# Kernel tuning notes

Hardware: AMD Instinct MI355X
Metric: run time of the kernel (lower is better)

## Reference

```python
import jax, jax.numpy as jnp
import numpy as np

N = 100000   # nodes
E = 300000   # directed edges
IN_DIM = 10
HID = 384
OUT_DIM = 3
T = 5
BN_EPS = 1e-5


def setup_inputs() -> dict:
    key = jax.random.key(0)
    ks = jax.random.split(key, 32)
    i = iter(range(32))
    nxt = lambda: ks[next(i)]
    d = {}
    d["x"] = jax.random.normal(nxt(), (N, IN_DIM), dtype=jnp.float32)
    d["edge_index"] = jax.random.randint(nxt(), (2, E), 0, N, dtype=jnp.int32)
    s = 0.05
    # SAGEConv layer 0 (in_dim -> hid); lin_l has bias, lin_r has no bias (PyG defaults)
    d["W_l0"] = jax.random.normal(nxt(), (HID, IN_DIM), dtype=jnp.float32) * s
    d["b_l0"] = jnp.zeros((HID,), dtype=jnp.float32)
    d["W_r0"] = jax.random.normal(nxt(), (HID, IN_DIM), dtype=jnp.float32) * s
    # SAGEConv layers 1..T-1 (hid -> hid), stacked
    d["W_l"] = jax.random.normal(nxt(), (T - 1, HID, HID), dtype=jnp.float32) * s
    d["b_l"] = jnp.zeros((T - 1, HID), dtype=jnp.float32)
    d["W_r"] = jax.random.normal(nxt(), (T - 1, HID, HID), dtype=jnp.float32) * s
    # per-layer BatchNorm (eval mode: running stats)
    d["bn_g"] = jnp.ones((T, HID), dtype=jnp.float32)
    d["bn_b"] = jnp.zeros((T, HID), dtype=jnp.float32)
    d["bn_m"] = jax.random.normal(nxt(), (T, HID), dtype=jnp.float32) * 0.1
    d["bn_v"] = jax.random.uniform(nxt(), (T, HID), dtype=jnp.float32, minval=0.5, maxval=1.5)
    # projection MLP: Linear->BN->ReLU->Linear->BN->ReLU->Linear
    d["Wp0"] = jax.random.normal(nxt(), (HID, HID), dtype=jnp.float32) * s
    d["bp0"] = jnp.zeros((HID,), dtype=jnp.float32)
    d["Wp1"] = jax.random.normal(nxt(), (HID, HID), dtype=jnp.float32) * s
    d["bp1"] = jnp.zeros((HID,), dtype=jnp.float32)
    d["Wp2"] = jax.random.normal(nxt(), (OUT_DIM, HID), dtype=jnp.float32) * s
    d["bp2"] = jnp.zeros((OUT_DIM,), dtype=jnp.float32)
    d["pbn_g"] = jnp.ones((2, HID), dtype=jnp.float32)
    d["pbn_b"] = jnp.zeros((2, HID), dtype=jnp.float32)
    d["pbn_m"] = jax.random.normal(nxt(), (2, HID), dtype=jnp.float32) * 0.1
    d["pbn_v"] = jax.random.uniform(nxt(), (2, HID), dtype=jnp.float32, minval=0.5, maxval=1.5)
    return d


def _bn(x, g, b, m, v):
    return (x - m) * jax.lax.rsqrt(v + BN_EPS) * g + b


def _sage(x, src, dst, Wl, bl, Wr):
    # mean aggregation of neighbor features, then lin_l(agg) + lin_r(x), L2-normalized
    msg = jax.ops.segment_sum(x[src], dst, num_segments=N)            # [N, F]
    cnt = jax.ops.segment_sum(jnp.ones_like(dst, dtype=x.dtype), dst, num_segments=N)
    agg = msg / jnp.maximum(cnt, 1.0)[:, None]
    out = agg @ Wl.T + bl + x @ Wr.T
    nrm = jnp.linalg.norm(out, axis=-1, keepdims=True)
    return out / jnp.maximum(nrm, 1e-12)


def reference(x, edge_index, W_l0, b_l0, W_r0, W_l, b_l, W_r,
              bn_g, bn_b, bn_m, bn_v,
              Wp0, bp0, Wp1, bp1, Wp2, bp2,
              pbn_g, pbn_b, pbn_m, pbn_v):
    src, dst = edge_index[0], edge_index[1]
    h = x
    for t in range(T):  # T=5, fixed small loop over structurally distinct layers
        if t == 0:
            h = _sage(h, src, dst, W_l0, b_l0, W_r0)
        else:
            h = _sage(h, src, dst, W_l[t - 1], b_l[t - 1], W_r[t - 1])
        h = jax.nn.elu(_bn(h, bn_g[t], bn_b[t], bn_m[t], bn_v[t]))
        # dropout is identity in eval mode
    # projection MLP
    h = jax.nn.relu(_bn(h @ Wp0.T + bp0, pbn_g[0], pbn_b[0], pbn_m[0], pbn_v[0]))
    h = jax.nn.relu(_bn(h @ Wp1.T + bp1, pbn_g[1], pbn_b[1], pbn_m[1], pbn_v[1]))
    return h @ Wp2.T + bp2  # [N, 3]
```

## Files before the change

### kernel.cpp

```cpp
#include <hip/hip_runtime.h>
#include <hip/hip_bf16.h>

#define N_NODES 100000
#define N_EDGES 300000
#define IN_DIM 10
#define HID 384
#define OUT_DIM 3
#define T_LAYERS 5
#define BN_EPS 1e-5f

typedef __attribute__((ext_vector_type(8))) short short8;
typedef __attribute__((ext_vector_type(4))) float floatx4;

__device__ __forceinline__ float bf16f(short v) {
  return __uint_as_float(((unsigned)(unsigned short)v) << 16);
}

__device__ __forceinline__ void gld_lds16(const void* g, void* l) {
  __builtin_amdgcn_global_load_lds(
      (const __attribute__((address_space(1))) void*)g,
      (__attribute__((address_space(3))) void*)l, 16, 0, 0);
}


__global__ void count_k(const int* __restrict__ dst, int* __restrict__ cnt, int E) {
  int e = blockIdx.x * blockDim.x + threadIdx.x;
  if (e < E) atomicAdd(&cnt[dst[e]], 1);
}

__global__ void scan_partial_k(const int* __restrict__ cnt, int* __restrict__ bsum, int n) {
  int t = threadIdx.x;
  int i = blockIdx.x * 1024 + t;
  int v = (i < n) ? cnt[i] : 0;
  #pragma unroll
  for (int off = 1; off < 64; off <<= 1) v += __shfl_xor(v, off);
  __shared__ int ws[16];
  if ((t & 63) == 0) ws[t >> 6] = v;
  __syncthreads();
  if (t == 0) {
    int s = 0;
    #pragma unroll
    for (int w = 0; w < 16; ++w) s += ws[w];
    bsum[blockIdx.x] = s;
  }
}

__global__ void scan_small_k(int* __restrict__ bsum, int P) {
  __shared__ int s[1024];
  int t = threadIdx.x;
  int v = (t < P) ? bsum[t] : 0;
  s[t] = v;
  __syncthreads();
  for (int off = 1; off < 1024; off <<= 1) {
    int add = (t >= off) ? s[t - off] : 0;
    __syncthreads();
    s[t] += add;
    __syncthreads();
  }
  if (t < P) bsum[t] = s[t] - v;
}

__global__ void scan_final_k(const int* __restrict__ cnt, const int* __restrict__ bsum,
                             int* __restrict__ row_off, int n) {
  int t = threadIdx.x, lane = t & 63, wv = t >> 6;
  int i = blockIdx.x * 1024 + t;
  int v = (i < n) ? cnt[i] : 0;
  int x = v;
  #pragma unroll
  for (int off = 1; off < 64; off <<= 1) {
    int y = __shfl_up(x, off);
    if (lane >= off) x += y;
  }
  __shared__ int ws[16];
  if (lane == 63) ws[wv] = x;
  __syncthreads();
  if (t == 0) {
    int a = 0;
    #pragma unroll
    for (int w = 0; w < 16; ++w) { int tmp = ws[w]; ws[w] = a; a += tmp; }
  }
  __syncthreads();
  int excl = (x - v) + ws[wv] + bsum[blockIdx.x];
  if (i <= n) row_off[i] = excl;
}

__global__ void fill_k(const int* __restrict__ src, const int* __restrict__ dst,
                       const int* __restrict__ row_off, int* __restrict__ cursor,
                       int* __restrict__ csr, int E) {
  int e = blockIdx.x * blockDim.x + threadIdx.x;
  if (e < E) {
    int d = dst[e];
    int pos = atomicAdd(&cursor[d], 1);
    csr[row_off[d] + pos] = src[e];
  }
}


__global__ void conv_k(const float* __restrict__ src, __hip_bfloat16* __restrict__ dst, int n) {
  int i = blockIdx.x * blockDim.x + threadIdx.x;
  if (i < n) dst[i] = __float2bfloat16(src[i]);
}

__global__ void pack0_k(const float* __restrict__ x, const float* __restrict__ agg10,
                        __hip_bfloat16* __restrict__ X2, int n) {
  int i = blockIdx.x * blockDim.x + threadIdx.x;
  if (i < n * 64) {
    int node = i >> 6, k = i & 63;
    float v = (k < IN_DIM) ? x[node * IN_DIM + k]
              : (k < 2 * IN_DIM) ? agg10[node * IN_DIM + (k - IN_DIM)] : 0.f;
    X2[i] = __float2bfloat16(v);
  }
}

__global__ void packw0_k(const float* __restrict__ Wl, const float* __restrict__ Wr,
                         __hip_bfloat16* __restrict__ W2) {
  int i = blockIdx.x * blockDim.x + threadIdx.x;
  if (i < HID * 64) {
    int o = i >> 6, k = i & 63;
    float v = (k < IN_DIM) ? Wr[o * IN_DIM + k]
              : (k < 2 * IN_DIM) ? Wl[o * IN_DIM + (k - IN_DIM)]
              : 0.f;
    W2[i] = __float2bfloat16(v);
  }
}


__global__ void agg10_k(const float* __restrict__ x, const int* __restrict__ row_off,
                        const int* __restrict__ csr, float* __restrict__ agg10, int n) {
  int sub = threadIdx.x >> 5;
  int lane = threadIdx.x & 31;
  int node = blockIdx.x * 8 + sub;
  if (node >= n) return;
  int s = row_off[node], e = row_off[node + 1];
  if (lane < IN_DIM) {
    float acc = 0.f;
    for (int j = s; j < e; ++j) acc += x[csr[j] * IN_DIM + lane];
    float c = (float)max(e - s, 1);
    agg10[node * IN_DIM + lane] = acc / c;
  }
}

__global__ __launch_bounds__(256) void aggv_k(const __hip_bfloat16* __restrict__ h,
                                              const int* __restrict__ row_off,
                                              const int* __restrict__ csr,
                                              __hip_bfloat16* __restrict__ agg, int n) {
  int node = blockIdx.x * 4 + (threadIdx.x >> 6);
  if (node >= n) return;
  int lane = threadIdx.x & 63;
  int s = row_off[node], e = row_off[node + 1];
  float a0 = 0.f, a1 = 0.f, a2 = 0.f, a3 = 0.f, a4 = 0.f, a5 = 0.f;
  const int doff = lane * 3;
  for (int j = s; j < e; ++j) {
    const uint* rp = (const uint*)(h + (size_t)csr[j] * HID) + doff;
    uint3 v = *(const uint3*)rp;
    a0 += __uint_as_float(v.x << 16);
    a1 += __uint_as_float(v.x & 0xffff0000u);
    a2 += __uint_as_float(v.y << 16);
    a3 += __uint_as_float(v.y & 0xffff0000u);
    a4 += __uint_as_float(v.z << 16);
    a5 += __uint_as_float(v.z & 0xffff0000u);
  }
  float invc = 1.f / (float)max(e - s, 1);
  __hip_bfloat16 b0 = __float2bfloat16(a0 * invc), b1 = __float2bfloat16(a1 * invc);
  __hip_bfloat16 b2 = __float2bfloat16(a2 * invc), b3 = __float2bfloat16(a3 * invc);
  __hip_bfloat16 b4 = __float2bfloat16(a4 * invc), b5 = __float2bfloat16(a5 * invc);
  uint o0 = (uint)(*(unsigned short*)&b0) | ((uint)(*(unsigned short*)&b1) << 16);
  uint o1 = (uint)(*(unsigned short*)&b2) | ((uint)(*(unsigned short*)&b3) << 16);
  uint o2 = (uint)(*(unsigned short*)&b4) | ((uint)(*(unsigned short*)&b5) << 16);
  *(uint3*)((uint*)(agg + (size_t)node * HID) + doff) = make_uint3(o0, o1, o2);
}

template <int KTOT, bool DUAL, int EPI, bool FINAL>
__global__ __launch_bounds__(512, 4) void mfma_gemm_k(
    const __hip_bfloat16* __restrict__ A1, const __hip_bfloat16* __restrict__ B1,
    const __hip_bfloat16* __restrict__ A2, const __hip_bfloat16* __restrict__ B2,
    const float* __restrict__ bias,
    const float* __restrict__ bng, const float* __restrict__ bnb,
    const float* __restrict__ bnm, const float* __restrict__ bnv,
    __hip_bfloat16* __restrict__ out,
    const float* __restrict__ W3, const float* __restrict__ b3,
    float* __restrict__ out3) {
  __shared__ alignas(16) short smem[32768];
  short* sB = smem + 8192;

  const int t = threadIdx.x;
  const int lane = t & 63;
  const int wv = t >> 6;
  const int n16 = lane & 15;
  const int quad = lane >> 4;
  const int row0 = blockIdx.x * 64;

  const int aRow = t >> 3;
  const int aG = (t & 7) ^ (aRow & 7);
  const int aOff = min(row0 + aRow, N_NODES - 1) * KTOT + aG * 8;
  const int bCol0 = wv * 48 + (lane >> 3);
  const int bG = (lane & 7) ^ ((lane >> 3) & 7);
  const int bOff0 = bCol0 * KTOT + bG * 8;

  floatx4 acc[4][3];
  #pragma unroll
  for (int rt = 0; rt < 4; ++rt)
    #pragma unroll
    for (int ct = 0; ct < 3; ++ct) acc[rt][ct] = (floatx4)0.f;

  constexpr int KCH = KTOT / 64;
  constexpr int NCH = DUAL ? 2 * KCH : KCH;

  gld_lds16(A1 + aOff, smem + wv * 512);

  for (int c = 0; c < NCH; ++c) {
    const __hip_bfloat16* Bp;
    int kc;
    if (!DUAL || c < KCH) { Bp = B1; kc = c * 64; }
    else                  { Bp = B2; kc = (c - KCH) * 64; }

    #pragma unroll
    for (int it = 0; it < 6; ++it)
      gld_lds16(Bp + bOff0 + (it * 8 * KTOT + kc), sB + (wv * 6 + it) * 512);

    if (c + 1 < NCH) {
      const __hip_bfloat16* Ap;
      int kn;
      int cn = c + 1;
      if (!DUAL || cn < KCH) { Ap = A1; kn = cn * 64; }
      else                   { Ap = A2; kn = (cn - KCH) * 64; }
      gld_lds16(Ap + aOff + kn, smem + (cn & 1) * 4096 + wv * 512);
      asm volatile("s_waitcnt vmcnt(1)" ::: "memory");
    } else {
      asm volatile("s_waitcnt vmcnt(0)" ::: "memory");
    }
    __builtin_amdgcn_sched_barrier(0);
    __builtin_amdgcn_s_barrier();

    const short* sAc = smem + (c & 1) * 4096;
    #pragma unroll
    for (int kh = 0; kh < 2; ++kh) {
      short8 af[4];
      int g = kh * 4 + quad;
      #pragma unroll
      for (int rt = 0; rt < 4; ++rt) {
        int r = rt * 16 + n16;
        af[rt] = *(const short8*)&sAc[r * 64 + ((g ^ (r & 7)) * 8)];
      }
      #pragma unroll
      for (int ct = 0; ct < 3; ++ct) {
        int cl = wv * 48 + ct * 16 + n16;
        short8 bf = *(const short8*)&sB[cl * 64 + ((g ^ (cl & 7)) * 8)];
        #pragma unroll
        for (int rt = 0; rt < 4; ++rt)
          acc[rt][ct] = __builtin_amdgcn_mfma_f32_16x16x32_bf16(af[rt], bf, acc[rt][ct], 0, 0, 0);
      }
    }
    __builtin_amdgcn_s_barrier();
    asm volatile("" ::: "memory");
  }

  const int gcBase = wv * 48 + n16;
  #pragma unroll
  for (int ct = 0; ct < 3; ++ct) {
    float bs = bias[gcBase + ct * 16];
    #pragma unroll
    for (int rt = 0; rt < 4; ++rt)
      #pragma unroll
      for (int rg = 0; rg < 4; ++rg) acc[rt][ct][rg] += bs;
  }

  if constexpr (EPI == 0) {
    float* red = (float*)smem;
    #pragma unroll
    for (int rt = 0; rt < 4; ++rt)
      #pragma unroll
      for (int rg = 0; rg < 4; ++rg) {
        float s = 0.f;
        #pragma unroll
        for (int ct = 0; ct < 3; ++ct) s += acc[rt][ct][rg] * acc[rt][ct][rg];
        #pragma unroll
        for (int off = 1; off < 16; off <<= 1) s += __shfl_xor(s, off);
        if (n16 == 0) red[wv * 64 + rt * 16 + quad * 4 + rg] = s;
      }
    __syncthreads();
    #pragma unroll
    for (int rt = 0; rt < 4; ++rt) {
      float inv[4];
      #pragma unroll
      for (int rg = 0; rg < 4; ++rg) {
        int rl = rt * 16 + quad * 4 + rg;
        float ss = 0.f;
        #pragma unroll
        for (int w = 0; w < 8; ++w) ss += red[w * 64 + rl];
        inv[rg] = rsqrtf(fmaxf(ss, 1e-24f));
      }
      #pragma unroll
      for (int ct = 0; ct < 3; ++ct)
        #pragma unroll
        for (int rg = 0; rg < 4; ++rg) acc[rt][ct][rg] *= inv[rg];
    }
    __syncthreads();
  }

  constexpr int OS = 392;
  short* sO = smem;
  #pragma unroll
  for (int ct = 0; ct < 3; ++ct) {
    int col = gcBase + ct * 16;
    float sc = bng[col] * rsqrtf(bnv[col] + BN_EPS);
    float sh = bnb[col] - bnm[col] * sc;
    #pragma unroll
    for (int rt = 0; rt < 4; ++rt)
      #pragma unroll
      for (int rg = 0; rg < 4; ++rg) {
        float xv = acc[rt][ct][rg] * sc + sh;
        if constexpr (EPI == 0)
          xv = xv > 0.f ? xv : (__expf(xv) - 1.0f);
        else
          xv = fmaxf(xv, 0.f);
        __hip_bfloat16 bv = __float2bfloat16(xv);
        sO[(rt * 16 + quad * 4 + rg) * OS + col] = *(short*)&bv;
      }
  }
  __syncthreads();

  if constexpr (FINAL) {
    if (t < 192) {
      int row = t & 63, o = t >> 6;
      int grow = row0 + row;
      if (grow < N_NODES) {
        float s = 0.f;
        #pragma unroll
        for (int kb = 0; kb < 48; ++kb) {
          short8 hv = *(const short8*)&sO[row * OS + kb * 8];
          #pragma unroll
          for (int j = 0; j < 8; ++j) s += bf16f(hv[j]) * W3[o * HID + kb * 8 + j];
        }
        out3[grow * OUT_DIM + o] = s + b3[o];
      }
    }
  } else {
    #pragma unroll
    for (int it = 0; it < 6; ++it) {
      int e = t + it * 512;
      int row = e / 48, cs = e % 48;
      int grow = row0 + row;
      if (grow < N_NODES) {
        uint4 v = *(const uint4*)&sO[row * OS + cs * 8];
        *(uint4*)(out + (size_t)grow * HID + cs * 8) = v;
      }
    }
  }
}


extern "C" void kernel_launch(void* const* d_in, const int* in_sizes, int n_in,
                              void* d_out, int out_size, void* d_ws, size_t ws_size,
                              hipStream_t stream) {
  const float* x = (const float*)d_in[0];
  const int* ei = (const int*)d_in[1];
  const int* src = ei;
  const int* dst = ei + N_EDGES;
  const float* W_l0 = (const float*)d_in[2];
  const float* b_l0 = (const float*)d_in[3];
  const float* W_r0 = (const float*)d_in[4];
  const float* W_l = (const float*)d_in[5];
  const float* b_l = (const float*)d_in[6];
  const float* W_r = (const float*)d_in[7];
  const float* bn_g = (const float*)d_in[8];
  const float* bn_b = (const float*)d_in[9];
  const float* bn_m = (const float*)d_in[10];
  const float* bn_v = (const float*)d_in[11];
  const float* Wp0 = (const float*)d_in[12];
  const float* bp0 = (const float*)d_in[13];
  const float* Wp1 = (const float*)d_in[14];
  const float* bp1 = (const float*)d_in[15];
  const float* Wp2 = (const float*)d_in[16];
  const float* bp2 = (const float*)d_in[17];
  const float* pbn_g = (const float*)d_in[18];
  const float* pbn_b = (const float*)d_in[19];
  const float* pbn_m = (const float*)d_in[20];
  const float* pbn_v = (const float*)d_in[21];

  char* ws = (char*)d_ws;
  size_t off = 0;
  auto walloc = [&](size_t bytes) -> void* {
    void* p = ws + off;
    off = (off + bytes + 255) & ~(size_t)255;
    return p;
  };
  __hip_bfloat16* h   = (__hip_bfloat16*)walloc((size_t)N_NODES * HID * 2);
  __hip_bfloat16* agg = (__hip_bfloat16*)walloc((size_t)N_NODES * HID * 2);
  float* agg10 = (float*)agg;
  __hip_bfloat16* X2  = (__hip_bfloat16*)walloc((size_t)N_NODES * 64 * 2);
  __hip_bfloat16* W2  = (__hip_bfloat16*)walloc((size_t)HID * 64 * 2);
  __hip_bfloat16* WlB  = (__hip_bfloat16*)walloc((size_t)(T_LAYERS - 1) * HID * HID * 2);
  __hip_bfloat16* WrB  = (__hip_bfloat16*)walloc((size_t)(T_LAYERS - 1) * HID * HID * 2);
  __hip_bfloat16* Wp0B = (__hip_bfloat16*)walloc((size_t)HID * HID * 2);
  __hip_bfloat16* Wp1B = (__hip_bfloat16*)walloc((size_t)HID * HID * 2);
  int* cnt     = (int*)walloc((size_t)N_NODES * 4);
  int* row_off = (int*)walloc((size_t)(N_NODES + 1) * 4);
  int* cursor  = (int*)walloc((size_t)N_NODES * 4);
  int* csr     = (int*)walloc((size_t)N_EDGES * 4);
  int* bsum    = (int*)walloc(4096);

  hipMemsetAsync(cnt, 0, (size_t)N_NODES * 4, stream);
  hipMemsetAsync(cursor, 0, (size_t)N_NODES * 4, stream);

  const int NW = (T_LAYERS - 1) * HID * HID;
  conv_k<<<(NW + 255) / 256, 256, 0, stream>>>(W_l, WlB, NW);
  conv_k<<<(NW + 255) / 256, 256, 0, stream>>>(W_r, WrB, NW);
  conv_k<<<(HID * HID + 255) / 256, 256, 0, stream>>>(Wp0, Wp0B, HID * HID);
  conv_k<<<(HID * HID + 255) / 256, 256, 0, stream>>>(Wp1, Wp1B, HID * HID);
  packw0_k<<<(HID * 64 + 255) / 256, 256, 0, stream>>>(W_l0, W_r0, W2);

  count_k<<<(N_EDGES + 255) / 256, 256, 0, stream>>>(dst, cnt, N_EDGES);
  int P = (N_NODES + 1 + 1023) / 1024;
  scan_partial_k<<<P, 1024, 0, stream>>>(cnt, bsum, N_NODES);
  scan_small_k<<<1, 1024, 0, stream>>>(bsum, P);
  scan_final_k<<<P, 1024, 0, stream>>>(cnt, bsum, row_off, N_NODES);
  fill_k<<<(N_EDGES + 255) / 256, 256, 0, stream>>>(src, dst, row_off, cursor, csr, N_EDGES);

  const int GB = (N_NODES + 63) / 64;

  agg10_k<<<(N_NODES + 7) / 8, 256, 0, stream>>>(x, row_off, csr, agg10, N_NODES);
  pack0_k<<<(N_NODES * 64 + 255) / 256, 256, 0, stream>>>(x, agg10, X2, N_NODES);
  mfma_gemm_k<64, false, 0, false><<<GB, 512, 0, stream>>>(
      X2, W2, nullptr, nullptr, b_l0, bn_g, bn_b, bn_m, bn_v, h,
      nullptr, nullptr, nullptr);

  for (int t = 1; t < T_LAYERS; ++t) {
    aggv_k<<<(N_NODES + 3) / 4, 256, 0, stream>>>(h, row_off, csr, agg, N_NODES);
    mfma_gemm_k<HID, true, 0, false><<<GB, 512, 0, stream>>>(
        agg, WlB + (size_t)(t - 1) * HID * HID,
        h,   WrB + (size_t)(t - 1) * HID * HID,
        b_l + (size_t)(t - 1) * HID,
        bn_g + (size_t)t * HID, bn_b + (size_t)t * HID,
        bn_m + (size_t)t * HID, bn_v + (size_t)t * HID,
        h, nullptr, nullptr, nullptr);
  }

  mfma_gemm_k<HID, false, 1, false><<<GB, 512, 0, stream>>>(
      h, Wp0B, nullptr, nullptr, bp0, pbn_g, pbn_b, pbn_m, pbn_v, h,
      nullptr, nullptr, nullptr);
  mfma_gemm_k<HID, false, 1, true><<<GB, 512, 0, stream>>>(
      h, Wp1B, nullptr, nullptr, bp1, pbn_g + HID, pbn_b + HID, pbn_m + HID, pbn_v + HID, h,
      Wp2, bp2, (float*)d_out);
}
```

Baseline: 910.2 us.

## Fuse projection MLP's two GEMMs and output layer into one kernel

Replaces the two separate projection GEMM launches with a single kernel that processes 128-row tiles with 1024 threads. The intermediate hidden activation stays in shared memory between the first GEMM, the second GEMM and the final 3-wide output. This removes a global write and re-read of the [N,384] bf16 intermediate and one launch. In exchange the kernel uses about 144 KB of LDS per block, which limits occupancy, and the second GEMM's B loads are not double-buffered.

```diff
diff --git a/kernel.cpp b/kernel.cpp
--- a/kernel.cpp
+++ b/kernel.cpp
@@ -345,6 +345,173 @@
         uint4 v = *(const uint4*)&sO[row * OS + cs * 8];
         *(uint4*)(out + (size_t)grow * HID + cs * 8) = v;
       }
+    }
+  }
+}
+
+__global__ __launch_bounds__(1024, 4) void proj_fused_k(
+    const __hip_bfloat16* __restrict__ h,
+    const __hip_bfloat16* __restrict__ B0, const __hip_bfloat16* __restrict__ B1,
+    const float* __restrict__ bias0, const float* __restrict__ bias1,
+    const float* __restrict__ pbn_g, const float* __restrict__ pbn_b,
+    const float* __restrict__ pbn_m, const float* __restrict__ pbn_v,
+    const float* __restrict__ W3, const float* __restrict__ b3,
+    float* __restrict__ out3) {
+  __shared__ alignas(16) short smem[73728];
+  short* sB = smem;
+  short* sA = smem + 24576;
+  short* sH = smem + 24576;
+
+  const int t = threadIdx.x;
+  const int lane = t & 63;
+  const int wv = t >> 6;
+  const int n16 = lane & 15;
+  const int quad = lane >> 4;
+  const int wr = wv >> 3, wc = wv & 7;
+  const int row0 = blockIdx.x * 128;
+
+  const int aRow = t >> 3;
+  const int aG = (t & 7) ^ (aRow & 7);
+  const size_t aOff = (size_t)min(row0 + aRow, N_NODES - 1) * HID + aG * 8;
+  const int bCol0 = wv * 24 + (lane >> 3);
+  const int bG = (lane & 7) ^ ((lane >> 3) & 7);
+  const int bOff0 = bCol0 * HID + bG * 8;
+
+  const int colBase = wc * 48 + n16;
+
+  floatx4 acc[4][3];
+  #pragma unroll
+  for (int rt = 0; rt < 4; ++rt)
+    #pragma unroll
+    for (int ct = 0; ct < 3; ++ct) acc[rt][ct] = (floatx4)0.f;
+
+  gld_lds16(h + aOff, sA + wv * 512);
+
+  for (int c = 0; c < 6; ++c) {
+    #pragma unroll
+    for (int it = 0; it < 3; ++it)
+      gld_lds16(B0 + bOff0 + (it * 8 * HID + c * 64), sB + (wv * 3 + it) * 512);
+    if (c + 1 < 6) {
+      gld_lds16(h + aOff + (c + 1) * 64, sA + ((c + 1) & 1) * 8192 + wv * 512);
+      asm volatile("s_waitcnt vmcnt(1)" ::: "memory");
+    } else {
+      asm volatile("s_waitcnt vmcnt(0)" ::: "memory");
+    }
+    __builtin_amdgcn_sched_barrier(0);
+    __builtin_amdgcn_s_barrier();
+
+    const short* sAc = sA + (c & 1) * 8192;
+    #pragma unroll
+    for (int kh = 0; kh < 2; ++kh) {
+      short8 af[4];
+      int g = kh * 4 + quad;
+      #pragma unroll
+      for (int rt = 0; rt < 4; ++rt) {
+        int r = wr * 64 + rt * 16 + n16;
+        af[rt] = *(const short8*)&sAc[r * 64 + ((g ^ (r & 7)) * 8)];
+      }
+      #pragma unroll
+      for (int ct = 0; ct < 3; ++ct) {
+        int cl = wc * 48 + ct * 16 + n16;
+        short8 bf = *(const short8*)&sB[cl * 64 + ((g ^ (cl & 7)) * 8)];
+        #pragma unroll
+        for (int rt = 0; rt < 4; ++rt)
+          acc[rt][ct] = __builtin_amdgcn_mfma_f32_16x16x32_bf16(af[rt], bf, acc[rt][ct], 0, 0, 0);
+      }
+    }
+    __builtin_amdgcn_s_barrier();
+    asm volatile("" ::: "memory");
+  }
+
+  __syncthreads();
+  #pragma unroll
+  for (int ct = 0; ct < 3; ++ct) {
+    int col = colBase + ct * 16;
+    float bs = bias0[col];
+    float sc = pbn_g[col] * rsqrtf(pbn_v[col] + BN_EPS);
+    float sh = pbn_b[col] - pbn_m[col] * sc;
+    #pragma unroll
+    for (int rt = 0; rt < 4; ++rt)
+      #pragma unroll
+      for (int rg = 0; rg < 4; ++rg) {
+        int row = wr * 64 + rt * 16 + quad * 4 + rg;
+        float xv = fmaxf((acc[rt][ct][rg] + bs) * sc + sh, 0.f);
+        __hip_bfloat16 bv = __float2bfloat16(xv);
+        sH[row * HID + ((col >> 6) << 6) + ((((col >> 3) & 7) ^ (row & 7)) * 8) + (col & 7)] =
+            *(short*)&bv;
+      }
+  }
+  __syncthreads();
+
+  #pragma unroll
+  for (int rt = 0; rt < 4; ++rt)
+    #pragma unroll
+    for (int ct = 0; ct < 3; ++ct) acc[rt][ct] = (floatx4)0.f;
+
+  for (int c = 0; c < 6; ++c) {
+    #pragma unroll
+    for (int it = 0; it < 3; ++it)
+      gld_lds16(B1 + bOff0 + (it * 8 * HID + c * 64), sB + (wv * 3 + it) * 512);
+    asm volatile("s_waitcnt vmcnt(0)" ::: "memory");
+    __builtin_amdgcn_sched_barrier(0);
+    __builtin_amdgcn_s_barrier();
+
+    const int kc = c * 64;
+    #pragma unroll
+    for (int kh = 0; kh < 2; ++kh) {
+      short8 af[4];
+      int g = kh * 4 + quad;
+      #pragma unroll
+      for (int rt = 0; rt < 4; ++rt) {
+        int r = wr * 64 + rt * 16 + n16;
+        af[rt] = *(const short8*)&sH[r * HID + kc + ((g ^ (n16 & 7)) * 8)];
+      }
+      #pragma unroll
+      for (int ct = 0; ct < 3; ++ct) {
+        int cl = wc * 48 + ct * 16 + n16;
+        short8 bf = *(const short8*)&sB[cl * 64 + ((g ^ (cl & 7)) * 8)];
+        #pragma unroll
+        for (int rt = 0; rt < 4; ++rt)
+          acc[rt][ct] = __builtin_amdgcn_mfma_f32_16x16x32_bf16(af[rt], bf, acc[rt][ct], 0, 0, 0);
+      }
+    }
+    __builtin_amdgcn_s_barrier();
+    asm volatile("" ::: "memory");
+  }
+
+  __syncthreads();
+  #pragma unroll
+  for (int ct = 0; ct < 3; ++ct) {
+    int col = colBase + ct * 16;
+    float bs = bias1[col];
+    float sc = pbn_g[HID + col] * rsqrtf(pbn_v[HID + col] + BN_EPS);
+    float sh = pbn_b[HID + col] - pbn_m[HID + col] * sc;
+    #pragma unroll
+    for (int rt = 0; rt < 4; ++rt)
+      #pragma unroll
+      for (int rg = 0; rg < 4; ++rg) {
+        int row = wr * 64 + rt * 16 + quad * 4 + rg;
+        float xv = fmaxf((acc[rt][ct][rg] + bs) * sc + sh, 0.f);
+        __hip_bfloat16 bv = __float2bfloat16(xv);
+        sH[row * HID + ((col >> 6) << 6) + ((((col >> 3) & 7) ^ (row & 7)) * 8) + (col & 7)] =
+            *(short*)&bv;
+      }
+  }
+  __syncthreads();
+
+  if (t < 384) {
+    int row = t & 127, o = t >> 7;
+    int grow = row0 + row;
+    if (grow < N_NODES) {
+      float s = 0.f;
+      #pragma unroll
+      for (int kb = 0; kb < 48; ++kb) {
+        short8 hv = *(const short8*)&sH[row * HID + ((kb >> 3) << 6) +
+                                        (((kb & 7) ^ (row & 7)) * 8)];
+        #pragma unroll
+        for (int j = 0; j < 8; ++j) s += bf16f(hv[j]) * W3[o * HID + kb * 8 + j];
+      }
+      out3[grow * OUT_DIM + o] = s + b3[o];
     }
   }
 }
@@ -418,6 +585,7 @@
   fill_k<<<(N_EDGES + 255) / 256, 256, 0, stream>>>(src, dst, row_off, cursor, csr, N_EDGES);
 
   const int GB = (N_NODES + 63) / 64;
+  const int GB2 = (N_NODES + 127) / 128;
 
   agg10_k<<<(N_NODES + 7) / 8, 256, 0, stream>>>(x, row_off, csr, agg10, N_NODES);
   pack0_k<<<(N_NODES * 64 + 255) / 256, 256, 0, stream>>>(x, agg10, X2, N_NODES);
@@ -436,10 +604,7 @@
         h, nullptr, nullptr, nullptr);
   }
 
-  mfma_gemm_k<HID, false, 1, false><<<GB, 512, 0, stream>>>(
-      h, Wp0B, nullptr, nullptr, bp0, pbn_g, pbn_b, pbn_m, pbn_v, h,
-      nullptr, nullptr, nullptr);
-  mfma_gemm_k<HID, false, 1, true><<<GB, 512, 0, stream>>>(
-      h, Wp1B, nullptr, nullptr, bp1, pbn_g + HID, pbn_b + HID, pbn_m + HID, pbn_v + HID, h,
+  proj_fused_k<<<GB2, 1024, 0, stream>>>(
+      h, Wp0B, Wp1B, bp0, bp1, pbn_g, pbn_b, pbn_m, pbn_v,
       Wp2, bp2, (float*)d_out);
 }
```

New measurement: 939.7 us. 1.03x slower.
